# Kernel tuning notes

Hardware: AMD Instinct MI355X
Metric: run time of the kernel (lower is better)

Reference implementation:

```python
import jax, jax.numpy as jnp
import numpy as np

N_NODES = 50000


def gcn_conv(x, edge_index, W, b, n_nodes):
    # GCNConv: h = x @ W; out_i = sum_{j->i} d_i^-1/2 d_j^-1/2 h_j + bias
    # with self-loops added (PyG defaults: add_self_loops=True, normalize=True).
    src, dst = edge_index[0], edge_index[1]
    loop = jnp.arange(n_nodes, dtype=src.dtype)
    src = jnp.concatenate([src, loop])
    dst = jnp.concatenate([dst, loop])
    deg = jax.ops.segment_sum(jnp.ones(src.shape, x.dtype), dst, num_segments=n_nodes)
    dinv = jnp.where(deg > 0, jax.lax.rsqrt(deg), 0.0)
    norm = dinv[src] * dinv[dst]            # [E+N]
    h = x @ W                                # [N, c_out] dense GEMM
    msg = h[src] * norm[:, None]             # [E+N, c_out] gather
    out = jax.ops.segment_sum(msg, dst, num_segments=n_nodes)  # scatter-add
    return out + b


def setup_inputs() -> dict:
    key = jax.random.key(0)
    k = jax.random.split(key, 4)
    c_in, c_out, E = 128, 128, 800000
    x = jax.random.normal(k[0], (N_NODES, c_in), jnp.float32)
    edge_index = jax.random.randint(k[1], (2, E), 0, N_NODES)
    W1 = jax.random.normal(k[2], (c_in, 2 * c_in), jnp.float32) / np.sqrt(c_in).astype(np.float32)
    b1 = jnp.zeros((2 * c_in,), jnp.float32)
    W2 = jax.random.normal(k[3], (2 * c_in, c_out), jnp.float32) / np.sqrt(2 * c_in).astype(np.float32)
    b2 = jnp.zeros((c_out,), jnp.float32)
    return {"x": x, "edge_index": edge_index, "W1": W1, "b1": b1, "W2": W2, "b2": b2}


def reference(x, edge_index, W1, b1, W2, b2):
    # eval mode: dropout is identity
    h = jax.nn.relu(gcn_conv(x, edge_index, W1, b1, N_NODES))
    out = jax.nn.relu(gcn_conv(h, edge_index, W2, b2, N_NODES))
    return out
```

## Files before the change

kernel.cpp:

```cpp
#include <hip/hip_runtime.h>


#define C_IN   128
#define C_HID  256
#define C_OUT  128
#define BKT    64

typedef __attribute__((ext_vector_type(8))) short short8;
typedef __attribute__((ext_vector_type(4))) short bfs4;
typedef __attribute__((ext_vector_type(4))) float floatx4;
typedef __attribute__((ext_vector_type(4))) float f32x4;
typedef __attribute__((ext_vector_type(2))) unsigned u32x2;

__device__ __forceinline__ unsigned short f2bf(float f) {
    unsigned u = __float_as_uint(f);
    u += 0x7FFFu + ((u >> 16) & 1u);
    return (unsigned short)(u >> 16);
}
__device__ __forceinline__ float bf2f(unsigned short b) {
    return __uint_as_float(((unsigned)b) << 16);
}
__device__ __forceinline__ unsigned pack_hilo(float f) {
    unsigned short hi = f2bf(f);
    unsigned short lo = f2bf(f - bf2f(hi));
    return ((unsigned)hi << 16) | (unsigned)lo;
}
__device__ __forceinline__ float bflo(unsigned v) {
    return __uint_as_float((v & 0xFFFFu) << 16);
}
__device__ __forceinline__ float bfhi(unsigned v) {
    return __uint_as_float(v & 0xFFFF0000u);
}

__global__ __launch_bounds__(256) void mega_pre(
        const int* __restrict__ src, const int* __restrict__ dst,
        int* __restrict__ cnt, unsigned short* __restrict__ buf16, int E, int n,
        const float* __restrict__ x, unsigned* __restrict__ xb2, int count4,
        const float* __restrict__ W1, unsigned* __restrict__ w1t,
        const float* __restrict__ W2, unsigned* __restrict__ w2t,
        int nb_fill, int nb_x, int nb_w1) {
    int b = blockIdx.x;
    int t = threadIdx.x;
    if (b < nb_fill) {
        int group = b & 7;
        int sub   = b >> 3;
        int nblk  = nb_fill >> 3;
        int chunk = (n + 7) / 8;
        int nlo = group * chunk;
        int nhi = min(n, nlo + chunk);
        int stride = nblk * 256;
        for (int e = sub * 256 + t; e < E; e += stride) {
            int d = dst[e];
            if (d >= nlo && d < nhi) {
                int s = src[e];
                int p = atomicAdd(&cnt[d], 1);
                if (p < BKT) buf16[(size_t)d * BKT + p] = (unsigned short)s;
            }
        }
    } else if (b < nb_fill + nb_x) {
        int idx = (b - nb_fill) * 256 + t;
        if (idx < count4) {
            f32x4 f = ((const f32x4*)x)[idx];
            unsigned lo = (unsigned)f2bf(f.x) | ((unsigned)f2bf(f.y) << 16);
            unsigned hi = (unsigned)f2bf(f.z) | ((unsigned)f2bf(f.w) << 16);
            u32x2 o; o.x = lo; o.y = hi;
            ((u32x2*)xb2)[idx] = o;
        }
    } else if (b < nb_fill + nb_x + nb_w1) {
        int idx = (b - nb_fill - nb_x) * 256 + t;
        if (idx < C_IN * C_HID) {
            int k = idx / C_HID, nn = idx - k * C_HID;
            w1t[(size_t)nn * C_IN + k] = pack_hilo(W1[idx]);
        }
    } else {
        int idx = (b - nb_fill - nb_x - nb_w1) * 256 + t;
        if (idx < C_HID * C_OUT) {
            int k = idx / C_OUT, nn = idx - k * C_OUT;
            w2t[(size_t)nn * C_HID + k] = pack_hilo(W2[idx]);
        }
    }
}

__global__ __launch_bounds__(256) void agg_kernel(
        const unsigned short* __restrict__ hb, const int* __restrict__ cnt,
        const unsigned short* __restrict__ buf16,
        const float* __restrict__ bias, float* __restrict__ out_f,
        unsigned* __restrict__ out_p, int relu_flag, int n) {
    int node = blockIdx.x * 4 + (threadIdx.x >> 6);
    if (node >= n) return;
    int lane = threadIdx.x & 63;

    const unsigned* hrow = (const unsigned*)hb;
    int cn = cnt[node];
    float di = rsqrtf((float)(cn + 1));
    unsigned sv = hrow[(size_t)node * 64 + lane];
    float a0 = di * bflo(sv);
    float a1 = di * bfhi(sv);

    int lo = node * BKT;
    int hi = lo + min(cn, BKT);

    unsigned short rec[8];
    #pragma unroll
    for (int u = 0; u < 8; ++u)
        rec[u] = buf16[lo + u];

    for (int k = lo; k < hi; k += 8) {
        int jj[8];
        #pragma unroll
        for (int u = 0; u < 8; ++u)
            jj[u] = ((k + u) < hi) ? (int)rec[u] : 0;
        int cj[8];
        #pragma unroll
        for (int u = 0; u < 8; ++u)
            cj[u] = cnt[jj[u]];
        unsigned v[8];
        #pragma unroll
        for (int u = 0; u < 8; ++u)
            v[u] = hrow[(size_t)jj[u] * 64 + lane];
        #pragma unroll
        for (int u = 0; u < 8; ++u)
            rec[u] = buf16[k + 8 + u];
        #pragma unroll
        for (int u = 0; u < 8; ++u) {
            float w = ((k + u) < hi) ? rsqrtf((float)(cj[u] + 1)) : 0.0f;
            a0 += w * bflo(v[u]);
            a1 += w * bfhi(v[u]);
        }
    }

    int c0 = lane * 2;
    float v0 = di * a0, v1f = di * a1;
    if (bias) { v0 += bias[c0]; v1f += bias[c0 + 1]; }
    if (relu_flag) { v0 = fmaxf(v0, 0.0f); v1f = fmaxf(v1f, 0.0f); }
    if (out_f) {
        unsigned long long ov = ((unsigned long long)__float_as_uint(v1f) << 32)
                              | (unsigned long long)__float_as_uint(v0);
        __builtin_nontemporal_store(ov, (unsigned long long*)(out_f + (size_t)node * 128 + c0));
    } else {
        unsigned long long ov = ((unsigned long long)pack_hilo(v1f) << 32)
                              | (unsigned long long)pack_hilo(v0);
        __builtin_nontemporal_store(ov, (unsigned long long*)(out_p + (size_t)node * 128 + c0));
    }
}

#define TM 32
#define TN 128
#define TK 32
#define LDK 40

__global__ __launch_bounds__(256) void mfma_gemm(
        const unsigned* __restrict__ Ap, const unsigned* __restrict__ Btp,
        const float* __restrict__ bias, float* __restrict__ Cf,
        unsigned* __restrict__ Cp, unsigned short* __restrict__ Cb,
        int M, int K, int N, int relu_flag) {
    __shared__ unsigned short smem[320 * LDK];
    unsigned short* As_hi = smem;
    unsigned short* As_lo = smem + 32 * LDK;
    unsigned short* Bs_hi = smem + 64 * LDK;
    unsigned short* Bs_lo = smem + 192 * LDK;

    int tid = threadIdx.x;
    int lane = tid & 63;
    int wv = tid >> 6;
    int n0w = wv * 32;
    int row0 = blockIdx.x * TM;
    int col0 = blockIdx.y * TN;

    int a_r  = tid >> 3;
    int a_kc = (tid & 7) * 4;
    int b_r  = tid >> 2;
    int b_kc = (tid & 3) * 8;

    floatx4 acc[2][2];
    #pragma unroll
    for (int i = 0; i < 2; ++i)
        #pragma unroll
        for (int j = 0; j < 2; ++j)
            acc[i][j] = (floatx4){0.f, 0.f, 0.f, 0.f};

    for (int k0 = 0; k0 < K; k0 += TK) {
        int ar = row0 + a_r;
        uint4 av = (ar < M) ? *(const uint4*)(Ap + (size_t)ar * K + k0 + a_kc)
                            : make_uint4(0, 0, 0, 0);
        uint4 bv[2][2];
        #pragma unroll
        for (int p = 0; p < 2; ++p) {
            const uint4* pb = (const uint4*)(Btp + (size_t)(col0 + b_r + p * 64) * K + k0 + b_kc);
            bv[p][0] = pb[0];  bv[p][1] = pb[1];
        }
        __syncthreads();
        {
            unsigned ua[4] = {av.x, av.y, av.z, av.w};
            bfs4 ah4, al4;
            #pragma unroll
            for (int j = 0; j < 4; ++j) {
                ah4[j] = (short)(ua[j] >> 16);  al4[j] = (short)(ua[j] & 0xFFFFu);
            }
            *(bfs4*)&As_hi[a_r * LDK + a_kc] = ah4;
            *(bfs4*)&As_lo[a_r * LDK + a_kc] = al4;
        }
        #pragma unroll
        for (int p = 0; p < 2; ++p) {
            int r = b_r + p * 64;
            unsigned ub[8] = {bv[p][0].x, bv[p][0].y, bv[p][0].z, bv[p][0].w,
                              bv[p][1].x, bv[p][1].y, bv[p][1].z, bv[p][1].w};
            short8 bhs, bls;
            #pragma unroll
            for (int j = 0; j < 8; ++j) {
                bhs[j] = (short)(ub[j] >> 16);  bls[j] = (short)(ub[j] & 0xFFFFu);
            }
            *(short8*)&Bs_hi[r * LDK + b_kc] = bhs;
            *(short8*)&Bs_lo[r * LDK + b_kc] = bls;
        }
        __syncthreads();
        short8 ah[2], al[2], bh[2], bl[2];
        int ka = (lane >> 4) * 8;
        #pragma unroll
        for (int mi = 0; mi < 2; ++mi) {
            int rr = mi * 16 + (lane & 15);
            ah[mi] = *(const short8*)&As_hi[rr * LDK + ka];
            al[mi] = *(const short8*)&As_lo[rr * LDK + ka];
        }
        #pragma unroll
        for (int ni = 0; ni < 2; ++ni) {
            int cc = n0w + ni * 16 + (lane & 15);
            bh[ni] = *(const short8*)&Bs_hi[cc * LDK + ka];
            bl[ni] = *(const short8*)&Bs_lo[cc * LDK + ka];
        }
        #pragma unroll
        for (int mi = 0; mi < 2; ++mi)
            #pragma unroll
            for (int ni = 0; ni < 2; ++ni) {
                acc[mi][ni] = __builtin_amdgcn_mfma_f32_16x16x32_bf16(al[mi], bh[ni], acc[mi][ni], 0, 0, 0);
                acc[mi][ni] = __builtin_amdgcn_mfma_f32_16x16x32_bf16(ah[mi], bl[ni], acc[mi][ni], 0, 0, 0);
                acc[mi][ni] = __builtin_amdgcn_mfma_f32_16x16x32_bf16(ah[mi], bh[ni], acc[mi][ni], 0, 0, 0);
            }
    }

    #pragma unroll
    for (int mi = 0; mi < 2; ++mi) {
        #pragma unroll
        for (int reg = 0; reg < 4; ++reg) {
            int r = row0 + mi * 16 + (lane >> 4) * 4 + reg;
            if (r < M) {
                #pragma unroll
                for (int ni = 0; ni < 2; ++ni) {
                    int c = col0 + n0w + ni * 16 + (lane & 15);
                    float v = acc[mi][ni][reg];
                    if (bias) v += bias[c];
                    if (relu_flag) v = fmaxf(v, 0.0f);
                    if (Cf)      Cf[(size_t)r * N + c] = v;
                    else if (Cp) Cp[(size_t)r * N + c] = pack_hilo(v);
                    else         Cb[(size_t)r * N + c] = f2bf(v);
                }
            }
        }
    }
}

extern "C" void kernel_launch(void* const* d_in, const int* in_sizes, int n_in,
                              void* d_out, int out_size, void* d_ws, size_t ws_size,
                              hipStream_t stream) {
    const float* x  = (const float*)d_in[0];
    const int*   ei = (const int*)d_in[1];
    const float* W1 = (const float*)d_in[2];
    const float* b1 = (const float*)d_in[3];
    const float* W2 = (const float*)d_in[4];
    const float* b2 = (const float*)d_in[5];

    const int n = in_sizes[0] / C_IN;
    const int E = in_sizes[1] / 2;

    const int* src = ei;
    const int* dst = ei + E;

    unsigned short* h2b = (unsigned short*)d_ws;
    unsigned* z1p = (unsigned*)(h2b + (size_t)n * C_OUT);
    unsigned short* xb = (unsigned short*)(z1p + (size_t)n * C_HID);
    unsigned* w1t = (unsigned*)(xb + (size_t)n * C_IN);
    unsigned* w2t = w1t + C_IN * C_HID;
    int* cnt = (int*)(w2t + C_HID * C_OUT);
    unsigned short* buf16 = (unsigned short*)(cnt + n);

    unsigned* agg0p = (unsigned*)d_out;
    float*    outp  = (float*)d_out;

    const int count4 = n * C_IN / 4;
    const int nblk_g = (E / 8 + 255) / 256;
    const int nb_fill = 8 * nblk_g;
    const int nb_x   = (count4 + 255) / 256;
    const int nb_w1  = (C_IN * C_HID + 255) / 256;
    const int nb_w2  = (C_HID * C_OUT + 255) / 256;

    hipMemsetAsync(cnt, 0, (size_t)n * sizeof(int), stream);
    mega_pre<<<nb_fill + nb_x + nb_w1 + nb_w2, 256, 0, stream>>>(
        src, dst, cnt, buf16, E, n,
        x, (unsigned*)xb, count4, W1, w1t, W2, w2t,
        nb_fill, nb_x, nb_w1);

    const int agg_blocks = (n + 3) / 4;

    agg_kernel<<<agg_blocks, 256, 0, stream>>>(xb, cnt, buf16,
                                               nullptr, nullptr, agg0p, 0, n);
    {
        dim3 grid((n + TM - 1) / TM, C_HID / TN);
        mfma_gemm<<<grid, 256, 0, stream>>>(agg0p, w1t, b1, nullptr, z1p, nullptr,
                                            n, C_IN, C_HID, 1);
    }

    {
        dim3 grid((n + TM - 1) / TM, C_OUT / TN);
        mfma_gemm<<<grid, 256, 0, stream>>>(z1p, w2t, nullptr, nullptr, nullptr, h2b,
                                            n, C_HID, C_OUT, 0);
    }
    agg_kernel<<<agg_blocks, 256, 0, stream>>>(h2b, cnt, buf16,
                                               b2, outp, nullptr, 1, n);
}
```

Before: 246.4 us.

## Split packed hi/lo bf16 operands into separate planar arrays and vectorize edge fill

Replaces the interleaved 32-bit hi/lo bf16 packing with separate hi and lo planes for weights, aggregated features and the hidden activations, so the GEMM loads go straight into LDS without per-element unpacking shifts. The producers (agg_kernel, mega_pre, GEMM epilogue) now write two planes with 16-bit stores. The edge bucket-fill loop also reads src/dst as int4 vectors when they are 16-byte aligned. Total bytes are unchanged. The cost is more, narrower stores in the GEMM epilogue.

```diff
diff --git a/kernel.cpp b/kernel.cpp
--- a/kernel.cpp
+++ b/kernel.cpp
@@ -11,6 +11,7 @@
 typedef __attribute__((ext_vector_type(4))) float floatx4;
 typedef __attribute__((ext_vector_type(4))) float f32x4;
 typedef __attribute__((ext_vector_type(2))) unsigned u32x2;
+typedef __attribute__((ext_vector_type(4))) int i32x4;
 
 __device__ __forceinline__ unsigned short f2bf(float f) {
     unsigned u = __float_as_uint(f);
@@ -20,11 +21,6 @@
 __device__ __forceinline__ float bf2f(unsigned short b) {
     return __uint_as_float(((unsigned)b) << 16);
 }
-__device__ __forceinline__ unsigned pack_hilo(float f) {
-    unsigned short hi = f2bf(f);
-    unsigned short lo = f2bf(f - bf2f(hi));
-    return ((unsigned)hi << 16) | (unsigned)lo;
-}
 __device__ __forceinline__ float bflo(unsigned v) {
     return __uint_as_float((v & 0xFFFFu) << 16);
 }
@@ -36,8 +32,10 @@
         const int* __restrict__ src, const int* __restrict__ dst,
         int* __restrict__ cnt, unsigned short* __restrict__ buf16, int E, int n,
         const float* __restrict__ x, unsigned* __restrict__ xb2, int count4,
-        const float* __restrict__ W1, unsigned* __restrict__ w1t,
-        const float* __restrict__ W2, unsigned* __restrict__ w2t,
+        const float* __restrict__ W1, unsigned short* __restrict__ w1h,
+        unsigned short* __restrict__ w1l,
+        const float* __restrict__ W2, unsigned short* __restrict__ w2h,
+        unsigned short* __restrict__ w2l,
         int nb_fill, int nb_x, int nb_w1) {
     int b = blockIdx.x;
     int t = threadIdx.x;
@@ -48,13 +46,38 @@
         int chunk = (n + 7) / 8;
         int nlo = group * chunk;
         int nhi = min(n, nlo + chunk);
-        int stride = nblk * 256;
-        for (int e = sub * 256 + t; e < E; e += stride) {
-            int d = dst[e];
-            if (d >= nlo && d < nhi) {
-                int s = src[e];
-                int p = atomicAdd(&cnt[d], 1);
-                if (p < BKT) buf16[(size_t)d * BKT + p] = (unsigned short)s;
+        int T = nblk * 256;
+        int g_tid = sub * 256 + t;
+        bool al16 = (((((size_t)dst) | ((size_t)src)) & 15) == 0);
+        if (al16) {
+            int E4 = E >> 2;
+            for (int v = g_tid; v < E4; v += T) {
+                i32x4 d4 = ((const i32x4*)dst)[v];
+                i32x4 s4 = ((const i32x4*)src)[v];
+                #pragma unroll
+                for (int u = 0; u < 4; ++u) {
+                    int d = d4[u];
+                    if (d >= nlo && d < nhi) {
+                        int p = atomicAdd(&cnt[d], 1);
+                        if (p < BKT) buf16[(size_t)d * BKT + p] = (unsigned short)s4[u];
+                    }
+                }
+            }
+            if (sub == 0 && t < (E & 3)) {
+                int e = (E4 << 2) + t;
+                int d = dst[e];
+                if (d >= nlo && d < nhi) {
+                    int p = atomicAdd(&cnt[d], 1);
+                    if (p < BKT) buf16[(size_t)d * BKT + p] = (unsigned short)src[e];
+                }
+            }
+        } else {
+            for (int e = g_tid; e < E; e += T) {
+                int d = dst[e];
+                if (d >= nlo && d < nhi) {
+                    int p = atomicAdd(&cnt[d], 1);
+                    if (p < BKT) buf16[(size_t)d * BKT + p] = (unsigned short)src[e];
+                }
             }
         }
     } else if (b < nb_fill + nb_x) {
@@ -70,13 +93,21 @@
         int idx = (b - nb_fill - nb_x) * 256 + t;
         if (idx < C_IN * C_HID) {
             int k = idx / C_HID, nn = idx - k * C_HID;
-            w1t[(size_t)nn * C_IN + k] = pack_hilo(W1[idx]);
+            float v = W1[idx];
+            unsigned short h = f2bf(v);
+            unsigned short l = f2bf(v - bf2f(h));
+            w1h[(size_t)nn * C_IN + k] = h;
+            w1l[(size_t)nn * C_IN + k] = l;
         }
     } else {
         int idx = (b - nb_fill - nb_x - nb_w1) * 256 + t;
         if (idx < C_HID * C_OUT) {
             int k = idx / C_OUT, nn = idx - k * C_OUT;
-            w2t[(size_t)nn * C_HID + k] = pack_hilo(W2[idx]);
+            float v = W2[idx];
+            unsigned short h = f2bf(v);
+            unsigned short l = f2bf(v - bf2f(h));
+            w2h[(size_t)nn * C_HID + k] = h;
+            w2l[(size_t)nn * C_HID + k] = l;
         }
     }
 }
@@ -85,7 +116,8 @@
         const unsigned short* __restrict__ hb, const int* __restrict__ cnt,
         const unsigned short* __restrict__ buf16,
         const float* __restrict__ bias, float* __restrict__ out_f,
-        unsigned* __restrict__ out_p, int relu_flag, int n) {
+        unsigned* __restrict__ out_h, unsigned* __restrict__ out_l,
+        int relu_flag, int n) {
     int node = blockIdx.x * 4 + (threadIdx.x >> 6);
     if (node >= n) return;
     int lane = threadIdx.x & 63;
@@ -138,9 +170,12 @@
                               | (unsigned long long)__float_as_uint(v0);
         __builtin_nontemporal_store(ov, (unsigned long long*)(out_f + (size_t)node * 128 + c0));
     } else {
-        unsigned long long ov = ((unsigned long long)pack_hilo(v1f) << 32)
-                              | (unsigned long long)pack_hilo(v0);
-        __builtin_nontemporal_store(ov, (unsigned long long*)(out_p + (size_t)node * 128 + c0));
+        unsigned short h0 = f2bf(v0), h1 = f2bf(v1f);
+        unsigned short l0 = f2bf(v0 - bf2f(h0)), l1 = f2bf(v1f - bf2f(h1));
+        unsigned hp = (unsigned)h0 | ((unsigned)h1 << 16);
+        unsigned lp = (unsigned)l0 | ((unsigned)l1 << 16);
+        __builtin_nontemporal_store(hp, out_h + (size_t)node * 64 + lane);
+        __builtin_nontemporal_store(lp, out_l + (size_t)node * 64 + lane);
     }
 }
 
@@ -150,9 +185,11 @@
 #define LDK 40
 
 __global__ __launch_bounds__(256) void mfma_gemm(
-        const unsigned* __restrict__ Ap, const unsigned* __restrict__ Btp,
-        const float* __restrict__ bias, float* __restrict__ Cf,
-        unsigned* __restrict__ Cp, unsigned short* __restrict__ Cb,
+        const unsigned short* __restrict__ Ah, const unsigned short* __restrict__ Al,
+        const unsigned short* __restrict__ Bh, const unsigned short* __restrict__ Bl,
+        const float* __restrict__ bias,
+        unsigned short* __restrict__ Ch, unsigned short* __restrict__ Cl,
+        unsigned short* __restrict__ Cb,
         int M, int K, int N, int relu_flag) {
     __shared__ unsigned short smem[320 * LDK];
     unsigned short* As_hi = smem;
@@ -181,37 +218,26 @@
 
     for (int k0 = 0; k0 < K; k0 += TK) {
         int ar = row0 + a_r;
-        uint4 av = (ar < M) ? *(const uint4*)(Ap + (size_t)ar * K + k0 + a_kc)
-                            : make_uint4(0, 0, 0, 0);
-        uint4 bv[2][2];
+        bfs4 avh = (bfs4){0,0,0,0}, avl = (bfs4){0,0,0,0};
+        if (ar < M) {
+            avh = *(const bfs4*)(Ah + (size_t)ar * K + k0 + a_kc);
+            avl = *(const bfs4*)(Al + (size_t)ar * K + k0 + a_kc);
+        }
+        short8 bvh[2], bvl[2];
         #pragma unroll
         for (int p = 0; p < 2; ++p) {
-            const uint4* pb = (const uint4*)(Btp + (size_t)(col0 + b_r + p * 64) * K + k0 + b_kc);
-            bv[p][0] = pb[0];  bv[p][1] = pb[1];
+            size_t roff = (size_t)(col0 + b_r + p * 64) * K + k0 + b_kc;
+            bvh[p] = *(const short8*)(Bh + roff);
+            bvl[p] = *(const short8*)(Bl + roff);
         }
         __syncthreads();
-        {
-            unsigned ua[4] = {av.x, av.y, av.z, av.w};
-            bfs4 ah4, al4;
-            #pragma unroll
-            for (int j = 0; j < 4; ++j) {
-                ah4[j] = (short)(ua[j] >> 16);  al4[j] = (short)(ua[j] & 0xFFFFu);
-            }
-            *(bfs4*)&As_hi[a_r * LDK + a_kc] = ah4;
-            *(bfs4*)&As_lo[a_r * LDK + a_kc] = al4;
-        }
+        *(bfs4*)&As_hi[a_r * LDK + a_kc] = avh;
+        *(bfs4*)&As_lo[a_r * LDK + a_kc] = avl;
         #pragma unroll
         for (int p = 0; p < 2; ++p) {
             int r = b_r + p * 64;
-            unsigned ub[8] = {bv[p][0].x, bv[p][0].y, bv[p][0].z, bv[p][0].w,
-                              bv[p][1].x, bv[p][1].y, bv[p][1].z, bv[p][1].w};
-            short8 bhs, bls;
-            #pragma unroll
-            for (int j = 0; j < 8; ++j) {
-                bhs[j] = (short)(ub[j] >> 16);  bls[j] = (short)(ub[j] & 0xFFFFu);
-            }
-            *(short8*)&Bs_hi[r * LDK + b_kc] = bhs;
-            *(short8*)&Bs_lo[r * LDK + b_kc] = bls;
+            *(short8*)&Bs_hi[r * LDK + b_kc] = bvh[p];
+            *(short8*)&Bs_lo[r * LDK + b_kc] = bvl[p];
         }
         __syncthreads();
         short8 ah[2], al[2], bh[2], bl[2];
@@ -250,9 +276,13 @@
                     float v = acc[mi][ni][reg];
                     if (bias) v += bias[c];
                     if (relu_flag) v = fmaxf(v, 0.0f);
-                    if (Cf)      Cf[(size_t)r * N + c] = v;
-                    else if (Cp) Cp[(size_t)r * N + c] = pack_hilo(v);
-                    else         Cb[(size_t)r * N + c] = f2bf(v);
+                    if (Cb) {
+                        Cb[(size_t)r * N + c] = f2bf(v);
+                    } else {
+                        unsigned short h = f2bf(v);
+                        Ch[(size_t)r * N + c] = h;
+                        Cl[(size_t)r * N + c] = f2bf(v - bf2f(h));
+                    }
                 }
             }
         }
@@ -276,15 +306,19 @@
     const int* dst = ei + E;
 
     unsigned short* h2b = (unsigned short*)d_ws;
-    unsigned* z1p = (unsigned*)(h2b + (size_t)n * C_OUT);
-    unsigned short* xb = (unsigned short*)(z1p + (size_t)n * C_HID);
-    unsigned* w1t = (unsigned*)(xb + (size_t)n * C_IN);
-    unsigned* w2t = w1t + C_IN * C_HID;
-    int* cnt = (int*)(w2t + C_HID * C_OUT);
+    unsigned short* z1h = h2b + (size_t)n * C_OUT;
+    unsigned short* z1l = z1h + (size_t)n * C_HID;
+    unsigned short* xb  = z1l + (size_t)n * C_HID;
+    unsigned short* w1h = xb + (size_t)n * C_IN;
+    unsigned short* w1l = w1h + C_IN * C_HID;
+    unsigned short* w2h = w1l + C_IN * C_HID;
+    unsigned short* w2l = w2h + C_HID * C_OUT;
+    int* cnt = (int*)(w2l + C_HID * C_OUT);
     unsigned short* buf16 = (unsigned short*)(cnt + n);
 
-    unsigned* agg0p = (unsigned*)d_out;
-    float*    outp  = (float*)d_out;
+    unsigned short* agg0h = (unsigned short*)d_out;
+    unsigned short* agg0l = agg0h + (size_t)n * C_IN;
+    float* outp = (float*)d_out;
 
     const int count4 = n * C_IN / 4;
     const int nblk_g = (E / 8 + 255) / 256;
@@ -296,24 +330,27 @@
     hipMemsetAsync(cnt, 0, (size_t)n * sizeof(int), stream);
     mega_pre<<<nb_fill + nb_x + nb_w1 + nb_w2, 256, 0, stream>>>(
         src, dst, cnt, buf16, E, n,
-        x, (unsigned*)xb, count4, W1, w1t, W2, w2t,
+        x, (unsigned*)xb, count4, W1, w1h, w1l, W2, w2h, w2l,
         nb_fill, nb_x, nb_w1);
 
     const int agg_blocks = (n + 3) / 4;
 
     agg_kernel<<<agg_blocks, 256, 0, stream>>>(xb, cnt, buf16,
-                                               nullptr, nullptr, agg0p, 0, n);
+                                               nullptr, nullptr,
+                                               (unsigned*)agg0h, (unsigned*)agg0l, 0, n);
     {
         dim3 grid((n + TM - 1) / TM, C_HID / TN);
-        mfma_gemm<<<grid, 256, 0, stream>>>(agg0p, w1t, b1, nullptr, z1p, nullptr,
+        mfma_gemm<<<grid, 256, 0, stream>>>(agg0h, agg0l, w1h, w1l, b1,
+                                            z1h, z1l, nullptr,
                                             n, C_IN, C_HID, 1);
     }
 
     {
         dim3 grid((n + TM - 1) / TM, C_OUT / TN);
-        mfma_gemm<<<grid, 256, 0, stream>>>(z1p, w2t, nullptr, nullptr, nullptr, h2b,
+        mfma_gemm<<<grid, 256, 0, stream>>>(z1h, z1l, w2h, w2l, nullptr,
+                                            nullptr, nullptr, h2b,
                                             n, C_HID, C_OUT, 0);
     }
     agg_kernel<<<agg_blocks, 256, 0, stream>>>(h2b, cnt, buf16,
-                                               b2, outp, nullptr, 1, n);
-}
+                                               b2, outp, nullptr, nullptr, 1, n);
+}
```

New measurement: 253.8 us. +3.0%, slower.

## Fuse the two dense GEMMs, keeping the hidden activation tile in shared memory

Applied to the files above, without the earlier changes.

Merges the layer-1 GEMM (with bias and ReLU) and the layer-2 GEMM into one kernel. Each 32-row block computes its 256-wide hidden tile, stores it as a hi/lo bf16 split in LDS, then multiplies it directly by W2. This removes the global write and re-read of the n×256 split-precision intermediate and one kernel launch. In exchange, LDS use per block rises substantially, which can lower occupancy, and the grid shrinks because the column-split dimension is gone.

```diff
diff --git a/kernel.cpp b/kernel.cpp
--- a/kernel.cpp
+++ b/kernel.cpp
@@ -144,87 +144,154 @@
     }
 }
 
-#define TM 32
-#define TN 128
-#define TK 32
+#define TM  32
+#define LDA 136
 #define LDK 40
-
-__global__ __launch_bounds__(256) void mfma_gemm(
-        const unsigned* __restrict__ Ap, const unsigned* __restrict__ Btp,
-        const float* __restrict__ bias, float* __restrict__ Cf,
-        unsigned* __restrict__ Cp, unsigned short* __restrict__ Cb,
-        int M, int K, int N, int relu_flag) {
-    __shared__ unsigned short smem[320 * LDK];
+#define LDZ 264
+
+__global__ __launch_bounds__(256) void mfma_gemm_fused(
+        const unsigned* __restrict__ Ap,
+        const unsigned* __restrict__ W1p,
+        const float* __restrict__ b1,
+        const unsigned* __restrict__ W2p,
+        unsigned short* __restrict__ H2,
+        int M) {
+    __shared__ unsigned short smem[(32 * LDA + 128 * LDK + 32 * LDZ) * 2];
     unsigned short* As_hi = smem;
-    unsigned short* As_lo = smem + 32 * LDK;
-    unsigned short* Bs_hi = smem + 64 * LDK;
-    unsigned short* Bs_lo = smem + 192 * LDK;
+    unsigned short* As_lo = As_hi + 32 * LDA;
+    unsigned short* Bs_hi = As_lo + 32 * LDA;
+    unsigned short* Bs_lo = Bs_hi + 128 * LDK;
+    unsigned short* Zs_hi = Bs_lo + 128 * LDK;
+    unsigned short* Zs_lo = Zs_hi + 32 * LDZ;
 
     int tid = threadIdx.x;
     int lane = tid & 63;
     int wv = tid >> 6;
     int n0w = wv * 32;
     int row0 = blockIdx.x * TM;
-    int col0 = blockIdx.y * TN;
 
     int a_r  = tid >> 3;
     int a_kc = (tid & 7) * 4;
     int b_r  = tid >> 2;
     int b_kc = (tid & 3) * 8;
 
-    floatx4 acc[2][2];
+    int ka = (lane >> 4) * 8;
+    int lr = lane & 15;
+
+    int ar = row0 + a_r;
+    #pragma unroll
+    for (int o = 0; o < 4; ++o) {
+        uint4 av = (ar < M) ? *(const uint4*)(Ap + (size_t)ar * C_IN + o * 32 + a_kc)
+                            : make_uint4(0, 0, 0, 0);
+        unsigned ua[4] = {av.x, av.y, av.z, av.w};
+        bfs4 h4, l4;
+        #pragma unroll
+        for (int j = 0; j < 4; ++j) {
+            h4[j] = (short)(ua[j] >> 16);  l4[j] = (short)(ua[j] & 0xFFFFu);
+        }
+        *(bfs4*)&As_hi[a_r * LDA + o * 32 + a_kc] = h4;
+        *(bfs4*)&As_lo[a_r * LDA + o * 32 + a_kc] = l4;
+    }
+
+    #pragma unroll 1
+    for (int nt = 0; nt < 2; ++nt) {
+        floatx4 acc[2][2];
+        #pragma unroll
+        for (int i = 0; i < 2; ++i)
+            #pragma unroll
+            for (int j = 0; j < 2; ++j)
+                acc[i][j] = (floatx4){0.f, 0.f, 0.f, 0.f};
+
+        for (int k0 = 0; k0 < C_IN; k0 += 32) {
+            #pragma unroll
+            for (int p = 0; p < 2; ++p) {
+                const uint4* pb = (const uint4*)(W1p + (size_t)(nt * 128 + b_r + p * 64) * C_IN + k0 + b_kc);
+                uint4 bv0 = pb[0], bv1 = pb[1];
+                unsigned ub[8] = {bv0.x, bv0.y, bv0.z, bv0.w, bv1.x, bv1.y, bv1.z, bv1.w};
+                short8 bhs, bls;
+                #pragma unroll
+                for (int j = 0; j < 8; ++j) {
+                    bhs[j] = (short)(ub[j] >> 16);  bls[j] = (short)(ub[j] & 0xFFFFu);
+                }
+                int r = b_r + p * 64;
+                *(short8*)&Bs_hi[r * LDK + b_kc] = bhs;
+                *(short8*)&Bs_lo[r * LDK + b_kc] = bls;
+            }
+            __syncthreads();
+            short8 ah[2], al[2], bh[2], bl[2];
+            #pragma unroll
+            for (int mi = 0; mi < 2; ++mi) {
+                int rr = mi * 16 + lr;
+                ah[mi] = *(const short8*)&As_hi[rr * LDA + k0 + ka];
+                al[mi] = *(const short8*)&As_lo[rr * LDA + k0 + ka];
+            }
+            #pragma unroll
+            for (int ni = 0; ni < 2; ++ni) {
+                int cc = n0w + ni * 16 + lr;
+                bh[ni] = *(const short8*)&Bs_hi[cc * LDK + ka];
+                bl[ni] = *(const short8*)&Bs_lo[cc * LDK + ka];
+            }
+            #pragma unroll
+            for (int mi = 0; mi < 2; ++mi)
+                #pragma unroll
+                for (int ni = 0; ni < 2; ++ni) {
+                    acc[mi][ni] = __builtin_amdgcn_mfma_f32_16x16x32_bf16(al[mi], bh[ni], acc[mi][ni], 0, 0, 0);
+                    acc[mi][ni] = __builtin_amdgcn_mfma_f32_16x16x32_bf16(ah[mi], bl[ni], acc[mi][ni], 0, 0, 0);
+                    acc[mi][ni] = __builtin_amdgcn_mfma_f32_16x16x32_bf16(ah[mi], bh[ni], acc[mi][ni], 0, 0, 0);
+                }
+            __syncthreads();
+        }
+        #pragma unroll
+        for (int mi = 0; mi < 2; ++mi) {
+            #pragma unroll
+            for (int reg = 0; reg < 4; ++reg) {
+                int r = mi * 16 + (lane >> 4) * 4 + reg;
+                #pragma unroll
+                for (int ni = 0; ni < 2; ++ni) {
+                    int c = nt * 128 + n0w + ni * 16 + lr;
+                    float v = acc[mi][ni][reg] + b1[c];
+                    v = fmaxf(v, 0.0f);
+                    unsigned short h = f2bf(v);
+                    Zs_hi[r * LDZ + c] = h;
+                    Zs_lo[r * LDZ + c] = f2bf(v - bf2f(h));
+                }
+            }
+        }
+    }
+
+    floatx4 acc2[2][2];
     #pragma unroll
     for (int i = 0; i < 2; ++i)
         #pragma unroll
         for (int j = 0; j < 2; ++j)
-            acc[i][j] = (floatx4){0.f, 0.f, 0.f, 0.f};
-
-    for (int k0 = 0; k0 < K; k0 += TK) {
-        int ar = row0 + a_r;
-        uint4 av = (ar < M) ? *(const uint4*)(Ap + (size_t)ar * K + k0 + a_kc)
-                            : make_uint4(0, 0, 0, 0);
-        uint4 bv[2][2];
+            acc2[i][j] = (floatx4){0.f, 0.f, 0.f, 0.f};
+
+    for (int k0 = 0; k0 < C_HID; k0 += 32) {
         #pragma unroll
         for (int p = 0; p < 2; ++p) {
-            const uint4* pb = (const uint4*)(Btp + (size_t)(col0 + b_r + p * 64) * K + k0 + b_kc);
-            bv[p][0] = pb[0];  bv[p][1] = pb[1];
-        }
-        __syncthreads();
-        {
-            unsigned ua[4] = {av.x, av.y, av.z, av.w};
-            bfs4 ah4, al4;
-            #pragma unroll
-            for (int j = 0; j < 4; ++j) {
-                ah4[j] = (short)(ua[j] >> 16);  al4[j] = (short)(ua[j] & 0xFFFFu);
-            }
-            *(bfs4*)&As_hi[a_r * LDK + a_kc] = ah4;
-            *(bfs4*)&As_lo[a_r * LDK + a_kc] = al4;
-        }
-        #pragma unroll
-        for (int p = 0; p < 2; ++p) {
-            int r = b_r + p * 64;
-            unsigned ub[8] = {bv[p][0].x, bv[p][0].y, bv[p][0].z, bv[p][0].w,
-                              bv[p][1].x, bv[p][1].y, bv[p][1].z, bv[p][1].w};
+            const uint4* pb = (const uint4*)(W2p + (size_t)(b_r + p * 64) * C_HID + k0 + b_kc);
+            uint4 bv0 = pb[0], bv1 = pb[1];
+            unsigned ub[8] = {bv0.x, bv0.y, bv0.z, bv0.w, bv1.x, bv1.y, bv1.z, bv1.w};
             short8 bhs, bls;
             #pragma unroll
             for (int j = 0; j < 8; ++j) {
                 bhs[j] = (short)(ub[j] >> 16);  bls[j] = (short)(ub[j] & 0xFFFFu);
             }
+            int r = b_r + p * 64;
             *(short8*)&Bs_hi[r * LDK + b_kc] = bhs;
             *(short8*)&Bs_lo[r * LDK + b_kc] = bls;
         }
         __syncthreads();
         short8 ah[2], al[2], bh[2], bl[2];
-        int ka = (lane >> 4) * 8;
         #pragma unroll
         for (int mi = 0; mi < 2; ++mi) {
-            int rr = mi * 16 + (lane & 15);
-            ah[mi] = *(const short8*)&As_hi[rr * LDK + ka];
-            al[mi] = *(const short8*)&As_lo[rr * LDK + ka];
+            int rr = mi * 16 + lr;
+            ah[mi] = *(const short8*)&Zs_hi[rr * LDZ + k0 + ka];
+            al[mi] = *(const short8*)&Zs_lo[rr * LDZ + k0 + ka];
         }
         #pragma unroll
         for (int ni = 0; ni < 2; ++ni) {
-            int cc = n0w + ni * 16 + (lane & 15);
+            int cc = n0w + ni * 16 + lr;
             bh[ni] = *(const short8*)&Bs_hi[cc * LDK + ka];
             bl[ni] = *(const short8*)&Bs_lo[cc * LDK + ka];
         }
@@ -232,10 +299,11 @@
         for (int mi = 0; mi < 2; ++mi)
             #pragma unroll
             for (int ni = 0; ni < 2; ++ni) {
-                acc[mi][ni] = __builtin_amdgcn_mfma_f32_16x16x32_bf16(al[mi], bh[ni], acc[mi][ni], 0, 0, 0);
-                acc[mi][ni] = __builtin_amdgcn_mfma_f32_16x16x32_bf16(ah[mi], bl[ni], acc[mi][ni], 0, 0, 0);
-                acc[mi][ni] = __builtin_amdgcn_mfma_f32_16x16x32_bf16(ah[mi], bh[ni], acc[mi][ni], 0, 0, 0);
-            }
+                acc2[mi][ni] = __builtin_amdgcn_mfma_f32_16x16x32_bf16(al[mi], bh[ni], acc2[mi][ni], 0, 0, 0);
+                acc2[mi][ni] = __builtin_amdgcn_mfma_f32_16x16x32_bf16(ah[mi], bl[ni], acc2[mi][ni], 0, 0, 0);
+                acc2[mi][ni] = __builtin_amdgcn_mfma_f32_16x16x32_bf16(ah[mi], bh[ni], acc2[mi][ni], 0, 0, 0);
+            }
+        __syncthreads();
     }
 
     #pragma unroll
@@ -246,13 +314,8 @@
             if (r < M) {
                 #pragma unroll
                 for (int ni = 0; ni < 2; ++ni) {
-                    int c = col0 + n0w + ni * 16 + (lane & 15);
-                    float v = acc[mi][ni][reg];
-                    if (bias) v += bias[c];
-                    if (relu_flag) v = fmaxf(v, 0.0f);
-                    if (Cf)      Cf[(size_t)r * N + c] = v;
-                    else if (Cp) Cp[(size_t)r * N + c] = pack_hilo(v);
-                    else         Cb[(size_t)r * N + c] = f2bf(v);
+                    int c = n0w + ni * 16 + lr;
+                    H2[(size_t)r * C_OUT + c] = f2bf(acc2[mi][ni][reg]);
                 }
             }
         }
@@ -276,8 +339,7 @@
     const int* dst = ei + E;
 
     unsigned short* h2b = (unsigned short*)d_ws;
-    unsigned* z1p = (unsigned*)(h2b + (size_t)n * C_OUT);
-    unsigned short* xb = (unsigned short*)(z1p + (size_t)n * C_HID);
+    unsigned short* xb  = h2b + (size_t)n * C_OUT;
     unsigned* w1t = (unsigned*)(xb + (size_t)n * C_IN);
     unsigned* w2t = w1t + C_IN * C_HID;
     int* cnt = (int*)(w2t + C_HID * C_OUT);
@@ -303,17 +365,10 @@
 
     agg_kernel<<<agg_blocks, 256, 0, stream>>>(xb, cnt, buf16,
                                                nullptr, nullptr, agg0p, 0, n);
-    {
-        dim3 grid((n + TM - 1) / TM, C_HID / TN);
-        mfma_gemm<<<grid, 256, 0, stream>>>(agg0p, w1t, b1, nullptr, z1p, nullptr,
-                                            n, C_IN, C_HID, 1);
-    }
-
-    {
-        dim3 grid((n + TM - 1) / TM, C_OUT / TN);
-        mfma_gemm<<<grid, 256, 0, stream>>>(z1p, w2t, nullptr, nullptr, nullptr, h2b,
-                                            n, C_HID, C_OUT, 0);
-    }
+
+    mfma_gemm_fused<<<(n + TM - 1) / TM, 256, 0, stream>>>(
+        agg0p, w1t, b1, w2t, h2b, n);
+
     agg_kernel<<<agg_blocks, 256, 0, stream>>>(h2b, cnt, buf16,
                                                b2, outp, nullptr, 1, n);
 }
```

New measurement: 247.2 us. About the same (+0.3%).
